# Optimization experiments

Hardware: AMD Instinct MI355X
Metric: run time of the kernel (lower is better)

## Reference

```python
import jax, jax.numpy as jnp
import numpy as np

# ----- problem dimensions (must match setup_inputs) -----
B = 50          # graphs per batch
NPG = 2000      # nodes per graph (equal-size graphs)
N = B * NPG     # total nodes = 100_000
D = 128         # in_channels
E = 600_000     # total edges
EA = 16         # edge_attr_dim
RATIO = 0.5
K = int(RATIO * NPG)  # nodes kept per graph = 1000
EPS = 1e-6


def setup_inputs() -> dict:
    key = jax.random.key(0)
    ks = jax.random.split(key, 12)
    x = jax.random.normal(ks[0], (N, D), jnp.float32)
    # edges constrained within graphs (each graph owns a contiguous node block)
    eg = jax.random.randint(ks[1], (E,), 0, B)
    src = eg * NPG + jax.random.randint(ks[2], (E,), 0, NPG)
    dst = eg * NPG + jax.random.randint(ks[3], (E,), 0, NPG)
    edge_index = jnp.stack([src, dst]).astype(jnp.int32)
    edge_attr = jax.random.normal(ks[4], (E, EA), jnp.float32)
    batch = (jnp.arange(N) // NPG).astype(jnp.int32)
    # feat_mlp: Linear(D,D) -> ReLU -> Linear(D,1)
    W1 = jax.random.normal(ks[5], (D, D), jnp.float32) / np.sqrt(D)
    b1 = jnp.zeros((D,), jnp.float32)
    W2 = jax.random.normal(ks[6], (D, 1), jnp.float32) / np.sqrt(D)
    b2 = jnp.zeros((1,), jnp.float32)
    # edge_mlp: Linear(EA,D) -> ReLU -> Linear(D,1)
    We1 = jax.random.normal(ks[7], (EA, D), jnp.float32) / np.sqrt(EA)
    be1 = jnp.zeros((D,), jnp.float32)
    We2 = jax.random.normal(ks[8], (D, 1), jnp.float32) / np.sqrt(D)
    be2 = jnp.zeros((1,), jnp.float32)
    view_weight = jnp.ones((3,), jnp.float32)
    return {"x": x, "edge_index": edge_index, "edge_attr": edge_attr,
            "batch": batch, "W1": W1, "b1": b1, "W2": W2, "b2": b2,
            "We1": We1, "be1": be1, "We2": We2, "be2": be2,
            "view_weight": view_weight}


def _standardize(v):
    # torch .std() is unbiased (ddof=1)
    return (v - v.mean()) / (jnp.std(v, ddof=1) + EPS)


def _scores(x, src, dst, edge_attr, W1, b1, W2, b2, We1, be1, We2, be2, vw):
    # edge weights: softplus(edge_mlp(edge_attr)) + eps
    ew = jax.nn.softplus((jax.nn.relu(edge_attr @ We1 + be1) @ We2 + be2)[:, 0]) + EPS
    deg_w = jnp.zeros((N,), x.dtype).at[src].add(ew)
    dis = jnp.where(deg_w > 0, deg_w ** -0.5, 0.0)
    norm = dis[src] * ew * dis[dst]                       # [E]
    x_diff = jnp.zeros_like(x).at[src].add(x[dst] * norm[:, None])  # [N,D]
    # view 1: structural (log degree)
    deg_c = jnp.zeros((N,), x.dtype).at[src].add(1.0)
    struct_score = _standardize(jnp.log(deg_c + 1.0))
    # view 2: feature MLP
    feat_raw = (jax.nn.relu(x @ W1 + b1) @ W2 + b2)[:, 0]
    feat_score = _standardize(feat_raw)
    # view 3: diffusion cosine similarity
    dot = jnp.sum(x * x_diff, axis=-1)
    cos = dot / ((jnp.linalg.norm(x, axis=-1) + EPS) *
                 (jnp.linalg.norm(x_diff, axis=-1) + EPS))
    diff_score = _standardize(cos)
    raw = jnp.stack([struct_score, feat_score, diff_score], axis=-1) @ vw
    return jax.nn.sigmoid(raw)                            # [N]


def reference(x, edge_index, edge_attr, batch, W1, b1, W2, b2,
              We1, be1, We2, be2, view_weight):
    src, dst = edge_index[0], edge_index[1]
    score = _scores(x, src, dst, edge_attr, W1, b1, W2, b2,
                    We1, be1, We2, be2, view_weight)
    # vectorized per-graph top-k (graphs are equal-size contiguous blocks)
    loc = jax.lax.top_k(score.reshape(B, NPG), K)[1]      # [B,K] local indices
    keep = (jnp.arange(B, dtype=loc.dtype)[:, None] * NPG + loc).reshape(-1)  # [B*K]
    node_mask = jnp.zeros((N,), bool).at[keep].set(True)
    new_id = jnp.full((N,), -1, jnp.int32).at[keep].set(
        jnp.arange(B * K, dtype=jnp.int32))
    e_mask = node_mask[src] & node_mask[dst]              # [E]
    out_edge_index = jnp.where(e_mask[None, :],
                               jnp.stack([new_id[src], new_id[dst]]), 0)
    out_edge_attr = jnp.where(e_mask[:, None], edge_attr, 0.0)
    out_x = x[keep] * score[keep][:, None]                # [B*K, D]
    out_batch = (jnp.arange(B * K) // K).astype(batch.dtype)
    return out_x, out_edge_index, out_edge_attr, out_batch, e_mask
```

## Files before the change

### kernel.cpp

```cpp
#include <hip/hip_runtime.h>
#include <math.h>

#define NN   100000
#define DD   128
#define EE   600000
#define EAD  16
#define BB   50
#define NPG  2000
#define KK   1000
#define NKEEP (BB*KK)

#define OFF_OEI    6400000
#define OFF_OEA    7600000
#define OFF_OBATCH 17200000
#define OFF_EMASK  17250000

#define NRED 240
#define SCAN_NB 98

#define EASTR 20
__global__ __launch_bounds__(256) void k_edge_mlp(
    const float* __restrict__ edge_attr, const int* __restrict__ src,
    const float* __restrict__ We1, const float* __restrict__ be1,
    const float* __restrict__ We2, const float* __restrict__ be2,
    float* __restrict__ ew, float* __restrict__ deg_w, float* __restrict__ deg_c)
{
    __shared__ float ea[256 * EASTR];
    __shared__ float wt[2048];
    __shared__ float b1s[128];
    __shared__ float w2s[128];
    int tid = threadIdx.x;
    int ebase = blockIdx.x * 256;

    if (tid < 128) {
        float tmp[16];
        #pragma unroll
        for (int k = 0; k < 16; k++) tmp[k] = We1[k * DD + tid];
        #pragma unroll
        for (int c = 0; c < 4; c++)
            *(float4*)(wt + tid * 16 + c * 4) =
                make_float4(tmp[4*c], tmp[4*c+1], tmp[4*c+2], tmp[4*c+3]);
        b1s[tid] = be1[tid];
        w2s[tid] = We2[tid];
    }
    #pragma unroll
    for (int it = 0; it < 4; it++) {
        int idx = tid + 256 * it;
        long long g = (long long)ebase * 4 + idx;
        long long maxg = (long long)EE * 4;
        if (g >= maxg) g = maxg - 1;
        float4 v = ((const float4*)edge_attr)[g];
        int le = idx >> 2, c = idx & 3;
        *(float4*)(ea + le * EASTR + c * 4) = v;
    }
    __syncthreads();

    float av[16];
    {
        const float* a = ea + tid * EASTR;
        float4 a0 = *(const float4*)(a);
        float4 a1 = *(const float4*)(a + 4);
        float4 a2 = *(const float4*)(a + 8);
        float4 a3 = *(const float4*)(a + 12);
        av[0]=a0.x; av[1]=a0.y; av[2]=a0.z; av[3]=a0.w;
        av[4]=a1.x; av[5]=a1.y; av[6]=a1.z; av[7]=a1.w;
        av[8]=a2.x; av[9]=a2.y; av[10]=a2.z; av[11]=a2.w;
        av[12]=a3.x; av[13]=a3.y; av[14]=a3.z; av[15]=a3.w;
    }

    float acc = 0.f;
    #pragma unroll 4
    for (int j = 0; j < DD; j++) {
        float4 w0 = *(const float4*)(wt + j * 16);
        float4 w1 = *(const float4*)(wt + j * 16 + 4);
        float4 w2 = *(const float4*)(wt + j * 16 + 8);
        float4 w3 = *(const float4*)(wt + j * 16 + 12);
        float h = b1s[j];
        h += av[0]*w0.x;  h += av[1]*w0.y;  h += av[2]*w0.z;  h += av[3]*w0.w;
        h += av[4]*w1.x;  h += av[5]*w1.y;  h += av[6]*w1.z;  h += av[7]*w1.w;
        h += av[8]*w2.x;  h += av[9]*w2.y;  h += av[10]*w2.z; h += av[11]*w2.w;
        h += av[12]*w3.x; h += av[13]*w3.y; h += av[14]*w3.z; h += av[15]*w3.w;
        acc += fmaxf(h, 0.f) * w2s[j];
    }

    int e = ebase + tid;
    if (e < EE) {
        float a = acc + be2[0];
        float sp = fmaxf(a, 0.f) + log1pf(expf(-fabsf(a)));
        float w = sp + 1e-6f;
        ew[e] = w;
        int s = src[e];
        atomicAdd(&deg_w[s], w);
        atomicAdd(&deg_c[s], 1.0f);
    }
}

__global__ __launch_bounds__(256) void k_dis(const float* __restrict__ deg_w,
                                             float* __restrict__ dis)
{
    int n = blockIdx.x * 256 + threadIdx.x;
    if (n >= NN) return;
    float d = deg_w[n];
    dis[n] = d > 0.f ? 1.f / sqrtf(d) : 0.f;
}

__global__ __launch_bounds__(1024) void k_scan_block(
    const float* __restrict__ deg_c, int* __restrict__ scanned,
    int* __restrict__ blocksums)
{
    __shared__ int s[1024];
    int i = blockIdx.x * 1024 + threadIdx.x;
    int c = (i < NN) ? (int)deg_c[i] : 0;
    s[threadIdx.x] = c;
    __syncthreads();
    for (int off = 1; off < 1024; off <<= 1) {
        int v = (threadIdx.x >= off) ? s[threadIdx.x - off] : 0;
        __syncthreads();
        s[threadIdx.x] += v;
        __syncthreads();
    }
    if (i < NN) scanned[i] = s[threadIdx.x] - c;
    if (threadIdx.x == 1023) blocksums[blockIdx.x] = s[1023];
}

__global__ __launch_bounds__(128) void k_scan_top(int* __restrict__ blocksums)
{
    __shared__ int s[128];
    int c = (threadIdx.x < SCAN_NB) ? blocksums[threadIdx.x] : 0;
    s[threadIdx.x] = c;
    __syncthreads();
    for (int off = 1; off < 128; off <<= 1) {
        int v = (threadIdx.x >= off) ? s[threadIdx.x - off] : 0;
        __syncthreads();
        s[threadIdx.x] += v;
        __syncthreads();
    }
    if (threadIdx.x < SCAN_NB) blocksums[threadIdx.x] = s[threadIdx.x] - c;
}

__global__ __launch_bounds__(256) void k_cursor(
    const int* __restrict__ scanned, const int* __restrict__ blocksums,
    int* __restrict__ rowstart, int* __restrict__ cur)
{
    int n = blockIdx.x * 256 + threadIdx.x;
    if (n >= NN) return;
    int st = scanned[n] + blocksums[n >> 10];
    rowstart[n] = st;
    cur[n] = st;
}

__global__ __launch_bounds__(256) void k_scatter(
    const int* __restrict__ src, const int* __restrict__ dst,
    const float* __restrict__ ew, const float* __restrict__ dis,
    int* __restrict__ cur, int* __restrict__ csr_dst, float* __restrict__ csr_w)
{
    int e = blockIdx.x * 256 + threadIdx.x;
    if (e >= EE) return;
    int s = src[e], d = dst[e];
    float w = dis[s] * ew[e] * dis[d];
    int pos = atomicAdd(&cur[s], 1);
    csr_dst[pos] = d;
    csr_w[pos] = w;
}

__global__ __launch_bounds__(256) void k_gather_cos(
    const int* __restrict__ rowstart, const float* __restrict__ deg_c,
    const int* __restrict__ csr_dst, const float* __restrict__ csr_w,
    const float* __restrict__ x, float* __restrict__ raw0, float* __restrict__ raw2)
{
    int blk = blockIdx.x;
    int node = ((blk & 7) * 3125 + (blk >> 3)) * 4 + (threadIdx.x >> 6);
    int lane = threadIdx.x & 63;
    if (node >= NN) return;
    int start = rowstart[node];
    int deg = (int)deg_c[node];
    const float2* xp = (const float2*)x;
    float2 xn = xp[(size_t)node * 64 + lane];
    float2 acc = {0.f, 0.f};
    for (int base = 0; base < deg; base += 64) {
        int rem = deg - base; if (rem > 64) rem = 64;
        int md = 0; float mw = 0.f;
        if (lane < rem) {
            md = csr_dst[start + base + lane];
            mw = csr_w[start + base + lane];
        }
        int e = 0;
        for (; e + 4 <= rem; e += 4) {
            int d0 = __shfl(md, e, 64),   d1 = __shfl(md, e+1, 64);
            int d2 = __shfl(md, e+2, 64), d3 = __shfl(md, e+3, 64);
            float w0 = __shfl(mw, e, 64),   w1 = __shfl(mw, e+1, 64);
            float w2 = __shfl(mw, e+2, 64), w3 = __shfl(mw, e+3, 64);
            float2 v0 = xp[(size_t)d0 * 64 + lane];
            float2 v1 = xp[(size_t)d1 * 64 + lane];
            float2 v2 = xp[(size_t)d2 * 64 + lane];
            float2 v3 = xp[(size_t)d3 * 64 + lane];
            acc.x += w0 * v0.x; acc.y += w0 * v0.y;
            acc.x += w1 * v1.x; acc.y += w1 * v1.y;
            acc.x += w2 * v2.x; acc.y += w2 * v2.y;
            acc.x += w3 * v3.x; acc.y += w3 * v3.y;
        }
        for (; e < rem; e++) {
            int d = __shfl(md, e, 64);
            float w = __shfl(mw, e, 64);
            float2 v = xp[(size_t)d * 64 + lane];
            acc.x += w * v.x; acc.y += w * v.y;
        }
    }
    float dot = xn.x * acc.x + xn.y * acc.y;
    float nx  = xn.x * xn.x + xn.y * xn.y;
    float nd  = acc.x * acc.x + acc.y * acc.y;
    #pragma unroll
    for (int off = 32; off; off >>= 1) {
        dot += __shfl_xor(dot, off, 64);
        nx  += __shfl_xor(nx,  off, 64);
        nd  += __shfl_xor(nd,  off, 64);
    }
    if (lane == 0) {
        raw2[node] = dot / ((sqrtf(nx) + 1e-6f) * (sqrtf(nd) + 1e-6f));
        raw0[node] = logf((float)deg + 1.0f);
    }
}

#define XSTR 132
__global__ __launch_bounds__(256) void k_node(
    const float* __restrict__ x,
    const float* __restrict__ W1, const float* __restrict__ b1,
    const float* __restrict__ W2, const float* __restrict__ b2,
    float* __restrict__ raw1)
{
    __shared__ float xs[64 * XSTR];
    int wave = threadIdx.x >> 6, lane = threadIdx.x & 63;
    int ng = lane >> 4, jg = lane & 15;
    int blockBase = blockIdx.x * 64;

    #pragma unroll
    for (int it = 0; it < 8; it++) {
        int s = threadIdx.x + 256 * it;
        int row = s >> 5, c4 = s & 31;
        int gn = blockBase + row; if (gn >= NN) gn = NN - 1;
        *(float4*)(xs + row * XSTR + c4 * 4) =
            *(const float4*)(x + (size_t)gn * DD + c4 * 4);
    }
    __syncthreads();

    const float* xw = xs + (wave * 16 + ng * 4) * XSTR;
    int j0 = jg * 8;
    float acc[4][8];
    #pragma unroll
    for (int i = 0; i < 4; i++)
        #pragma unroll
        for (int jj = 0; jj < 8; jj++) acc[i][jj] = 0.f;

    for (int k = 0; k < DD; k += 4) {
        float4 xv[4];
        #pragma unroll
        for (int i = 0; i < 4; i++) xv[i] = *(const float4*)(xw + i * XSTR + k);
        float4 wv[4][2];
        #pragma unroll
        for (int kk = 0; kk < 4; kk++) {
            wv[kk][0] = *(const float4*)(W1 + (k + kk) * DD + j0);
            wv[kk][1] = *(const float4*)(W1 + (k + kk) * DD + j0 + 4);
        }
        #pragma unroll
        for (int i = 0; i < 4; i++) {
            const float xe[4] = {xv[i].x, xv[i].y, xv[i].z, xv[i].w};
            #pragma unroll
            for (int kk = 0; kk < 4; kk++) {
                acc[i][0] += xe[kk] * wv[kk][0].x;
                acc[i][1] += xe[kk] * wv[kk][0].y;
                acc[i][2] += xe[kk] * wv[kk][0].z;
                acc[i][3] += xe[kk] * wv[kk][0].w;
                acc[i][4] += xe[kk] * wv[kk][1].x;
                acc[i][5] += xe[kk] * wv[kk][1].y;
                acc[i][6] += xe[kk] * wv[kk][1].z;
                acc[i][7] += xe[kk] * wv[kk][1].w;
            }
        }
    }

    float4 b1a = *(const float4*)(b1 + j0), b1b = *(const float4*)(b1 + j0 + 4);
    float4 w2a = *(const float4*)(W2 + j0), w2b = *(const float4*)(W2 + j0 + 4);
    const float b1v[8] = {b1a.x,b1a.y,b1a.z,b1a.w, b1b.x,b1b.y,b1b.z,b1b.w};
    const float w2v[8] = {w2a.x,w2a.y,w2a.z,w2a.w, w2b.x,w2b.y,w2b.z,w2b.w};
    float bias2 = b2[0];
    #pragma unroll
    for (int i = 0; i < 4; i++) {
        float p = 0.f;
        #pragma unroll
        for (int jj = 0; jj < 8; jj++)
            p += fmaxf(acc[i][jj] + b1v[jj], 0.f) * w2v[jj];
        p += __shfl_xor(p, 1, 64);
        p += __shfl_xor(p, 2, 64);
        p += __shfl_xor(p, 4, 64);
        p += __shfl_xor(p, 8, 64);
        int node = blockBase + wave * 16 + ng * 4 + i;
        if (jg == 0 && node < NN) raw1[node] = p + bias2;
    }
}

__global__ __launch_bounds__(256) void k_reduce(
    const float* __restrict__ r0, const float* __restrict__ r1,
    const float* __restrict__ r2, double* __restrict__ partials)
{
    __shared__ double sd[256];
    double s[6] = {0,0,0,0,0,0};
    for (int n = blockIdx.x * 256 + threadIdx.x; n < NN; n += 256 * NRED) {
        double v0 = r0[n], v1 = r1[n], v2 = r2[n];
        s[0] += v0; s[1] += v0*v0;
        s[2] += v1; s[3] += v1*v1;
        s[4] += v2; s[5] += v2*v2;
    }
    for (int q = 0; q < 6; q++) {
        sd[threadIdx.x] = s[q];
        __syncthreads();
        for (int off = 128; off; off >>= 1) {
            if (threadIdx.x < off) sd[threadIdx.x] += sd[threadIdx.x + off];
            __syncthreads();
        }
        if (threadIdx.x == 0) partials[blockIdx.x * 6 + q] = sd[0];
        __syncthreads();
    }
}

__global__ __launch_bounds__(256) void k_stats(const double* __restrict__ partials,
                                               float* __restrict__ stats)
{
    __shared__ double sd[256];
    __shared__ double sums[6];
    for (int q = 0; q < 6; q++) {
        sd[threadIdx.x] = (threadIdx.x < NRED) ? partials[threadIdx.x * 6 + q] : 0.0;
        __syncthreads();
        for (int off = 128; off; off >>= 1) {
            if (threadIdx.x < off) sd[threadIdx.x] += sd[threadIdx.x + off];
            __syncthreads();
        }
        if (threadIdx.x == 0) sums[q] = sd[0];
        __syncthreads();
    }
    if (threadIdx.x == 0) {
        for (int i = 0; i < 3; i++) {
            double sum = sums[2*i], sq = sums[2*i+1];
            double mean = sum / NN;
            double var = (sq - sum * sum / NN) / (NN - 1);
            double sdv = sqrt(var > 0 ? var : 0);
            stats[2*i]   = (float)mean;
            stats[2*i+1] = (float)(1.0 / (sdv + 1e-6));
        }
    }
}

__global__ __launch_bounds__(256) void k_score(
    const float* __restrict__ r0, const float* __restrict__ r1,
    const float* __restrict__ r2, const float* __restrict__ stats,
    const float* __restrict__ vw, float* __restrict__ score)
{
    int n = blockIdx.x * 256 + threadIdx.x;
    if (n >= NN) return;
    float z0 = (r0[n] - stats[0]) * stats[1];
    float z1 = (r1[n] - stats[2]) * stats[3];
    float z2 = (r2[n] - stats[4]) * stats[5];
    float r = z0 * vw[0] + z1 * vw[1] + z2 * vw[2];
    score[n] = 1.f / (1.f + expf(-r));
}

__global__ __launch_bounds__(1024) void k_topk(
    const float* __restrict__ score, int* __restrict__ keep,
    int* __restrict__ new_id, float* __restrict__ obatch)
{
    __shared__ unsigned long long keys[2048];
    int b = blockIdx.x;
    unsigned t = threadIdx.x;
    for (unsigned i = t; i < 2048; i += 1024) {
        unsigned long long kk = 0ull;
        if (i < NPG) {
            float sc = score[b * NPG + i];
            kk = ((unsigned long long)__float_as_uint(sc) << 32)
               | (unsigned long long)(0xFFFFFFFFu - i);
        }
        keys[i] = kk;
    }
    __syncthreads();
    for (unsigned k = 2; k <= 2048; k <<= 1) {
        for (unsigned j = k >> 1; j > 0; j >>= 1) {
            unsigned i = ((t & ~(j - 1)) << 1) | (t & (j - 1));
            unsigned p = i | j;
            unsigned long long a = keys[i], c = keys[p];
            bool up = ((i & k) == 0);
            if ((a < c) == up) { keys[i] = c; keys[p] = a; }
            __syncthreads();
        }
    }
    if (t < KK) {
        unsigned long long kk = keys[t];
        unsigned li = 0xFFFFFFFFu - (unsigned)(kk & 0xFFFFFFFFu);
        int node = b * NPG + (int)li;
        int j = b * KK + (int)t;
        keep[j] = node;
        new_id[node] = j;
        obatch[j] = (float)b;
    }
}

__global__ __launch_bounds__(128) void k_outx(
    const float* __restrict__ x, const float* __restrict__ score,
    const int* __restrict__ keep, float* __restrict__ out_x)
{
    int j = blockIdx.x;
    int node = keep[j];
    float s = score[node];
    out_x[(size_t)j * DD + threadIdx.x] = x[(size_t)node * DD + threadIdx.x] * s;
}

__global__ __launch_bounds__(256) void k_edges(
    const int* __restrict__ src, const int* __restrict__ dst,
    const int* __restrict__ new_id, float* __restrict__ oei,
    float* __restrict__ emask)
{
    int e = blockIdx.x * 256 + threadIdx.x;
    if (e >= EE) return;
    int ns = new_id[src[e]], nd = new_id[dst[e]];
    bool m = (ns >= 0) && (nd >= 0);
    oei[e]      = m ? (float)ns : 0.f;
    oei[EE + e] = m ? (float)nd : 0.f;
    emask[e]    = m ? 1.f : 0.f;
}

__global__ __launch_bounds__(256) void k_attr(
    const float* __restrict__ edge_attr, const float* __restrict__ emask,
    float* __restrict__ oea)
{
    int idx = blockIdx.x * 256 + threadIdx.x;
    if (idx >= EE * 4) return;
    int e = idx >> 2;
    float m = emask[e];
    float4 v = ((const float4*)edge_attr)[idx];
    float4 o; o.x = v.x*m; o.y = v.y*m; o.z = v.z*m; o.w = v.w*m;
    ((float4*)oea)[idx] = o;
}

extern "C" void kernel_launch(void* const* d_in, const int* in_sizes, int n_in,
                              void* d_out, int out_size, void* d_ws, size_t ws_size,
                              hipStream_t stream) {
    const float* x         = (const float*)d_in[0];
    const int*   edge_idx  = (const int*)d_in[1];
    const float* edge_attr = (const float*)d_in[2];
    const float* W1  = (const float*)d_in[4];
    const float* b1  = (const float*)d_in[5];
    const float* W2  = (const float*)d_in[6];
    const float* b2  = (const float*)d_in[7];
    const float* We1 = (const float*)d_in[8];
    const float* be1 = (const float*)d_in[9];
    const float* We2 = (const float*)d_in[10];
    const float* be2 = (const float*)d_in[11];
    const float* vw  = (const float*)d_in[12];

    const int* src = edge_idx;
    const int* dst = edge_idx + EE;

    float* out    = (float*)d_out;
    float* out_x  = out;
    float* oei    = out + OFF_OEI;
    float* oea    = out + OFF_OEA;
    float* obatch = out + OFF_OBATCH;
    float* emask  = out + OFF_EMASK;

    int*   csr_dst   = (int*)(out + 12800000);
    float* csr_w     = out + 13400000;
    int*   rowstart  = (int*)(out + 14000000);
    int*   cur       = (int*)(out + 14100000);
    int*   scanned   = (int*)(out + 14200000);
    int*   blocksums = (int*)(out + 14300000);

    float* ws     = (float*)d_ws;
    float* ew     = ws;
    float* deg_w  = ws + 600000;
    float* deg_c  = ws + 700000;
    float* dis    = ws + 800000;
    float* score  = ws + 900000;
    float* raw0   = ws + 1000000;
    float* raw1   = ws + 1100000;
    float* raw2   = ws + 1200000;
    int*   keep   = (int*)(ws + 1300000);
    int*   new_id = (int*)(ws + 1350000);
    double* partials = (double*)(ws + 1450000);
    float* stats  = ws + 1450000 + 2 * 6 * NRED;

    hipMemsetAsync(deg_w, 0, 2 * NN * sizeof(float), stream);
    hipMemsetAsync(new_id, 0xFF, NN * sizeof(int), stream);

    k_edge_mlp<<<(EE + 255) / 256, 256, 0, stream>>>(edge_attr, src, We1, be1,
                                                     We2, be2, ew, deg_w, deg_c);
    k_dis<<<(NN + 255) / 256, 256, 0, stream>>>(deg_w, dis);
    k_scan_block<<<SCAN_NB, 1024, 0, stream>>>(deg_c, scanned, blocksums);
    k_scan_top<<<1, 128, 0, stream>>>(blocksums);
    k_cursor<<<(NN + 255) / 256, 256, 0, stream>>>(scanned, blocksums, rowstart, cur);
    k_scatter<<<(EE + 255) / 256, 256, 0, stream>>>(src, dst, ew, dis, cur, csr_dst, csr_w);
    k_gather_cos<<<(NN * 64 + 255) / 256, 256, 0, stream>>>(rowstart, deg_c, csr_dst,
                                                            csr_w, x, raw0, raw2);
    k_node<<<(NN + 63) / 64, 256, 0, stream>>>(x, W1, b1, W2, b2, raw1);
    k_reduce<<<NRED, 256, 0, stream>>>(raw0, raw1, raw2, partials);
    k_stats<<<1, 256, 0, stream>>>(partials, stats);
    k_score<<<(NN + 255) / 256, 256, 0, stream>>>(raw0, raw1, raw2, stats, vw, score);
    k_topk<<<BB, 1024, 0, stream>>>(score, keep, new_id, obatch);
    k_outx<<<NKEEP, 128, 0, stream>>>(x, score, keep, out_x);
    k_edges<<<(EE + 255) / 256, 256, 0, stream>>>(src, dst, new_id, oei, emask);
    k_attr<<<(EE * 4 + 255) / 256, 256, 0, stream>>>(edge_attr, emask, oea);
}
```

Baseline: 430.4 us.

## Pre-pack edge MLP weights and compute two edges per thread from global

A tiny prep kernel packs We1 columns, be1 and We2 into a 20-float-per-hidden-unit layout in scratch output memory. The edge MLP kernel then drops its shared-memory staging and reads these weights directly from global, where all lanes hit the same address and the cache serves them. Each thread now handles two edges, so every weight fetch feeds twice as many FMAs. This trades shared-memory staging and barrier cost for higher register pressure and one extra kernel launch.

New measurement: 444.6 us. +3.3%, slower.

```diff
diff --git a/kernel.cpp b/kernel.cpp
--- a/kernel.cpp
+++ b/kernel.cpp
@@ -18,78 +18,83 @@
 #define NRED 240
 #define SCAN_NB 98
 
-#define EASTR 20
+__global__ __launch_bounds__(128) void k_wprep(
+    const float* __restrict__ We1, const float* __restrict__ be1,
+    const float* __restrict__ We2, float* __restrict__ wp)
+{
+    int j = threadIdx.x;
+    #pragma unroll
+    for (int k = 0; k < EAD; k++) wp[j * 20 + k] = We1[k * DD + j];
+    wp[j * 20 + 16] = be1[j];
+    wp[j * 20 + 17] = We2[j];
+    wp[j * 20 + 18] = 0.f;
+    wp[j * 20 + 19] = 0.f;
+}
+
 __global__ __launch_bounds__(256) void k_edge_mlp(
     const float* __restrict__ edge_attr, const int* __restrict__ src,
-    const float* __restrict__ We1, const float* __restrict__ be1,
-    const float* __restrict__ We2, const float* __restrict__ be2,
+    const float* __restrict__ wp, const float* __restrict__ be2,
     float* __restrict__ ew, float* __restrict__ deg_w, float* __restrict__ deg_c)
 {
-    __shared__ float ea[256 * EASTR];
-    __shared__ float wt[2048];
-    __shared__ float b1s[128];
-    __shared__ float w2s[128];
     int tid = threadIdx.x;
-    int ebase = blockIdx.x * 256;
-
-    if (tid < 128) {
-        float tmp[16];
-        #pragma unroll
-        for (int k = 0; k < 16; k++) tmp[k] = We1[k * DD + tid];
-        #pragma unroll
-        for (int c = 0; c < 4; c++)
-            *(float4*)(wt + tid * 16 + c * 4) =
-                make_float4(tmp[4*c], tmp[4*c+1], tmp[4*c+2], tmp[4*c+3]);
-        b1s[tid] = be1[tid];
-        w2s[tid] = We2[tid];
-    }
-    #pragma unroll
-    for (int it = 0; it < 4; it++) {
-        int idx = tid + 256 * it;
-        long long g = (long long)ebase * 4 + idx;
-        long long maxg = (long long)EE * 4;
-        if (g >= maxg) g = maxg - 1;
-        float4 v = ((const float4*)edge_attr)[g];
-        int le = idx >> 2, c = idx & 3;
-        *(float4*)(ea + le * EASTR + c * 4) = v;
-    }
-    __syncthreads();
-
-    float av[16];
-    {
-        const float* a = ea + tid * EASTR;
-        float4 a0 = *(const float4*)(a);
-        float4 a1 = *(const float4*)(a + 4);
-        float4 a2 = *(const float4*)(a + 8);
-        float4 a3 = *(const float4*)(a + 12);
-        av[0]=a0.x; av[1]=a0.y; av[2]=a0.z; av[3]=a0.w;
-        av[4]=a1.x; av[5]=a1.y; av[6]=a1.z; av[7]=a1.w;
-        av[8]=a2.x; av[9]=a2.y; av[10]=a2.z; av[11]=a2.w;
-        av[12]=a3.x; av[13]=a3.y; av[14]=a3.z; av[15]=a3.w;
-    }
-
-    float acc = 0.f;
+    int ebase = blockIdx.x * 512;
+    int e0 = ebase + tid;
+    int e1 = ebase + 256 + tid;
+    int le0 = (e0 < EE) ? e0 : (EE - 1);
+    int le1 = (e1 < EE) ? e1 : (EE - 1);
+
+    const float4* ea4 = (const float4*)edge_attr;
+    float a0[16], a1[16];
+    #pragma unroll
+    for (int c = 0; c < 4; c++) {
+        float4 v = ea4[(size_t)le0 * 4 + c];
+        a0[4*c] = v.x; a0[4*c+1] = v.y; a0[4*c+2] = v.z; a0[4*c+3] = v.w;
+    }
+    #pragma unroll
+    for (int c = 0; c < 4; c++) {
+        float4 v = ea4[(size_t)le1 * 4 + c];
+        a1[4*c] = v.x; a1[4*c+1] = v.y; a1[4*c+2] = v.z; a1[4*c+3] = v.w;
+    }
+
+    float acc0 = 0.f, acc1 = 0.f;
     #pragma unroll 4
     for (int j = 0; j < DD; j++) {
-        float4 w0 = *(const float4*)(wt + j * 16);
-        float4 w1 = *(const float4*)(wt + j * 16 + 4);
-        float4 w2 = *(const float4*)(wt + j * 16 + 8);
-        float4 w3 = *(const float4*)(wt + j * 16 + 12);
-        float h = b1s[j];
-        h += av[0]*w0.x;  h += av[1]*w0.y;  h += av[2]*w0.z;  h += av[3]*w0.w;
-        h += av[4]*w1.x;  h += av[5]*w1.y;  h += av[6]*w1.z;  h += av[7]*w1.w;
-        h += av[8]*w2.x;  h += av[9]*w2.y;  h += av[10]*w2.z; h += av[11]*w2.w;
-        h += av[12]*w3.x; h += av[13]*w3.y; h += av[14]*w3.z; h += av[15]*w3.w;
-        acc += fmaxf(h, 0.f) * w2s[j];
-    }
-
-    int e = ebase + tid;
-    if (e < EE) {
-        float a = acc + be2[0];
+        const float* w = wp + j * 20;
+        float4 w0 = *(const float4*)(w);
+        float4 w1 = *(const float4*)(w + 4);
+        float4 w2 = *(const float4*)(w + 8);
+        float4 w3 = *(const float4*)(w + 12);
+        float bj  = w[16];
+        float v2  = w[17];
+        float h0 = bj, h1 = bj;
+        h0 += a0[0]*w0.x;  h0 += a0[1]*w0.y;  h0 += a0[2]*w0.z;  h0 += a0[3]*w0.w;
+        h0 += a0[4]*w1.x;  h0 += a0[5]*w1.y;  h0 += a0[6]*w1.z;  h0 += a0[7]*w1.w;
+        h0 += a0[8]*w2.x;  h0 += a0[9]*w2.y;  h0 += a0[10]*w2.z; h0 += a0[11]*w2.w;
+        h0 += a0[12]*w3.x; h0 += a0[13]*w3.y; h0 += a0[14]*w3.z; h0 += a0[15]*w3.w;
+        h1 += a1[0]*w0.x;  h1 += a1[1]*w0.y;  h1 += a1[2]*w0.z;  h1 += a1[3]*w0.w;
+        h1 += a1[4]*w1.x;  h1 += a1[5]*w1.y;  h1 += a1[6]*w1.z;  h1 += a1[7]*w1.w;
+        h1 += a1[8]*w2.x;  h1 += a1[9]*w2.y;  h1 += a1[10]*w2.z; h1 += a1[11]*w2.w;
+        h1 += a1[12]*w3.x; h1 += a1[13]*w3.y; h1 += a1[14]*w3.z; h1 += a1[15]*w3.w;
+        acc0 += fmaxf(h0, 0.f) * v2;
+        acc1 += fmaxf(h1, 0.f) * v2;
+    }
+
+    float bias2 = be2[0];
+    if (e0 < EE) {
+        float a = acc0 + bias2;
         float sp = fmaxf(a, 0.f) + log1pf(expf(-fabsf(a)));
         float w = sp + 1e-6f;
-        ew[e] = w;
-        int s = src[e];
+        ew[e0] = w;
+        int s = src[e0];
+        atomicAdd(&deg_w[s], w);
+        atomicAdd(&deg_c[s], 1.0f);
+    }
+    if (e1 < EE) {
+        float a = acc1 + bias2;
+        float sp = fmaxf(a, 0.f) + log1pf(expf(-fabsf(a)));
+        float w = sp + 1e-6f;
+        ew[e1] = w;
+        int s = src[e1];
         atomicAdd(&deg_w[s], w);
         atomicAdd(&deg_c[s], 1.0f);
     }
@@ -470,6 +475,7 @@
     int*   cur       = (int*)(out + 14100000);
     int*   scanned   = (int*)(out + 14200000);
     int*   blocksums = (int*)(out + 14300000);
+    float* wp        = out + 14400000;
 
     float* ws     = (float*)d_ws;
     float* ew     = ws;
@@ -488,8 +494,9 @@
     hipMemsetAsync(deg_w, 0, 2 * NN * sizeof(float), stream);
     hipMemsetAsync(new_id, 0xFF, NN * sizeof(int), stream);
 
-    k_edge_mlp<<<(EE + 255) / 256, 256, 0, stream>>>(edge_attr, src, We1, be1,
-                                                     We2, be2, ew, deg_w, deg_c);
+    k_wprep<<<1, 128, 0, stream>>>(We1, be1, We2, wp);
+    k_edge_mlp<<<(EE + 511) / 512, 256, 0, stream>>>(edge_attr, src, wp, be2,
+                                                     ew, deg_w, deg_c);
     k_dis<<<(NN + 255) / 256, 256, 0, stream>>>(deg_w, dis);
     k_scan_block<<<SCAN_NB, 1024, 0, stream>>>(deg_c, scanned, blocksums);
     k_scan_top<<<1, 128, 0, stream>>>(blocksums);
```

## Register-tile edge MLP across lanes with shuffle reduction over hidden units

Applied to the files above, without the earlier changes.

Rewrites the edge MLP kernel so each block handles 64 edges. Each lane computes a 4-edge by 8-hidden-unit register tile, reading weights straight from global/L1 instead of staging the whole weight matrix in shared memory, and the output dot product is reduced across 16 lanes with shuffles. This cuts the redundant per-thread 128x16 loop and the heavy shared-memory weight reads, but launches four times more blocks and adds shuffle and partial-lane work.

Result: no change. 434.1 us (+0.8%).

```diff
diff --git a/kernel.cpp b/kernel.cpp
--- a/kernel.cpp
+++ b/kernel.cpp
@@ -18,80 +18,89 @@
 #define NRED 240
 #define SCAN_NB 98
 
-#define EASTR 20
+#define EB 64
 __global__ __launch_bounds__(256) void k_edge_mlp(
     const float* __restrict__ edge_attr, const int* __restrict__ src,
     const float* __restrict__ We1, const float* __restrict__ be1,
     const float* __restrict__ We2, const float* __restrict__ be2,
     float* __restrict__ ew, float* __restrict__ deg_w, float* __restrict__ deg_c)
 {
-    __shared__ float ea[256 * EASTR];
-    __shared__ float wt[2048];
-    __shared__ float b1s[128];
-    __shared__ float w2s[128];
+    __shared__ float ea[EB * 20];
     int tid = threadIdx.x;
-    int ebase = blockIdx.x * 256;
-
-    if (tid < 128) {
-        float tmp[16];
-        #pragma unroll
-        for (int k = 0; k < 16; k++) tmp[k] = We1[k * DD + tid];
-        #pragma unroll
-        for (int c = 0; c < 4; c++)
-            *(float4*)(wt + tid * 16 + c * 4) =
-                make_float4(tmp[4*c], tmp[4*c+1], tmp[4*c+2], tmp[4*c+3]);
-        b1s[tid] = be1[tid];
-        w2s[tid] = We2[tid];
-    }
+    int wave = tid >> 6, lane = tid & 63;
+    int ng = lane >> 4, jg = lane & 15;
+    int ebase = blockIdx.x * EB;
+
+    {
+        int row = tid >> 2, c = tid & 3;
+        *(float4*)(ea + row * 20 + c * 4) =
+            *(const float4*)(edge_attr + (size_t)(ebase + row) * EAD + c * 4);
+    }
+    __syncthreads();
+
+    int j0 = jg * 8;
+    const float* xw = ea + (wave * 16 + ng * 4) * 20;
+
+    float acc[4][8];
     #pragma unroll
-    for (int it = 0; it < 4; it++) {
-        int idx = tid + 256 * it;
-        long long g = (long long)ebase * 4 + idx;
-        long long maxg = (long long)EE * 4;
-        if (g >= maxg) g = maxg - 1;
-        float4 v = ((const float4*)edge_attr)[g];
-        int le = idx >> 2, c = idx & 3;
-        *(float4*)(ea + le * EASTR + c * 4) = v;
-    }
-    __syncthreads();
-
-    float av[16];
-    {
-        const float* a = ea + tid * EASTR;
-        float4 a0 = *(const float4*)(a);
-        float4 a1 = *(const float4*)(a + 4);
-        float4 a2 = *(const float4*)(a + 8);
-        float4 a3 = *(const float4*)(a + 12);
-        av[0]=a0.x; av[1]=a0.y; av[2]=a0.z; av[3]=a0.w;
-        av[4]=a1.x; av[5]=a1.y; av[6]=a1.z; av[7]=a1.w;
-        av[8]=a2.x; av[9]=a2.y; av[10]=a2.z; av[11]=a2.w;
-        av[12]=a3.x; av[13]=a3.y; av[14]=a3.z; av[15]=a3.w;
-    }
-
-    float acc = 0.f;
-    #pragma unroll 4
-    for (int j = 0; j < DD; j++) {
-        float4 w0 = *(const float4*)(wt + j * 16);
-        float4 w1 = *(const float4*)(wt + j * 16 + 4);
-        float4 w2 = *(const float4*)(wt + j * 16 + 8);
-        float4 w3 = *(const float4*)(wt + j * 16 + 12);
-        float h = b1s[j];
-        h += av[0]*w0.x;  h += av[1]*w0.y;  h += av[2]*w0.z;  h += av[3]*w0.w;
-        h += av[4]*w1.x;  h += av[5]*w1.y;  h += av[6]*w1.z;  h += av[7]*w1.w;
-        h += av[8]*w2.x;  h += av[9]*w2.y;  h += av[10]*w2.z; h += av[11]*w2.w;
-        h += av[12]*w3.x; h += av[13]*w3.y; h += av[14]*w3.z; h += av[15]*w3.w;
-        acc += fmaxf(h, 0.f) * w2s[j];
-    }
-
-    int e = ebase + tid;
-    if (e < EE) {
-        float a = acc + be2[0];
-        float sp = fmaxf(a, 0.f) + log1pf(expf(-fabsf(a)));
-        float w = sp + 1e-6f;
-        ew[e] = w;
-        int s = src[e];
-        atomicAdd(&deg_w[s], w);
-        atomicAdd(&deg_c[s], 1.0f);
+    for (int i = 0; i < 4; i++)
+        #pragma unroll
+        for (int jj = 0; jj < 8; jj++) acc[i][jj] = 0.f;
+
+    #pragma unroll 1
+    for (int k = 0; k < EAD; k += 4) {
+        float4 xv[4];
+        #pragma unroll
+        for (int i = 0; i < 4; i++) xv[i] = *(const float4*)(xw + i * 20 + k);
+        float4 wv[4][2];
+        #pragma unroll
+        for (int kk = 0; kk < 4; kk++) {
+            wv[kk][0] = *(const float4*)(We1 + (k + kk) * DD + j0);
+            wv[kk][1] = *(const float4*)(We1 + (k + kk) * DD + j0 + 4);
+        }
+        #pragma unroll
+        for (int i = 0; i < 4; i++) {
+            const float xe[4] = {xv[i].x, xv[i].y, xv[i].z, xv[i].w};
+            #pragma unroll
+            for (int kk = 0; kk < 4; kk++) {
+                acc[i][0] += xe[kk] * wv[kk][0].x;
+                acc[i][1] += xe[kk] * wv[kk][0].y;
+                acc[i][2] += xe[kk] * wv[kk][0].z;
+                acc[i][3] += xe[kk] * wv[kk][0].w;
+                acc[i][4] += xe[kk] * wv[kk][1].x;
+                acc[i][5] += xe[kk] * wv[kk][1].y;
+                acc[i][6] += xe[kk] * wv[kk][1].z;
+                acc[i][7] += xe[kk] * wv[kk][1].w;
+            }
+        }
+    }
+
+    float4 b1a = *(const float4*)(be1 + j0), b1b = *(const float4*)(be1 + j0 + 4);
+    float4 w2a = *(const float4*)(We2 + j0), w2b = *(const float4*)(We2 + j0 + 4);
+    const float b1v[8] = {b1a.x,b1a.y,b1a.z,b1a.w, b1b.x,b1b.y,b1b.z,b1b.w};
+    const float w2v[8] = {w2a.x,w2a.y,w2a.z,w2a.w, w2b.x,w2b.y,w2b.z,w2b.w};
+    float bias2 = be2[0];
+
+    #pragma unroll
+    for (int i = 0; i < 4; i++) {
+        float p = 0.f;
+        #pragma unroll
+        for (int jj = 0; jj < 8; jj++)
+            p += fmaxf(acc[i][jj] + b1v[jj], 0.f) * w2v[jj];
+        p += __shfl_xor(p, 1, 64);
+        p += __shfl_xor(p, 2, 64);
+        p += __shfl_xor(p, 4, 64);
+        p += __shfl_xor(p, 8, 64);
+        if (jg == 0) {
+            int e = ebase + wave * 16 + ng * 4 + i;
+            float a = p + bias2;
+            float sp = fmaxf(a, 0.f) + log1pf(expf(-fabsf(a)));
+            float w = sp + 1e-6f;
+            ew[e] = w;
+            int s = src[e];
+            atomicAdd(&deg_w[s], w);
+            atomicAdd(&deg_c[s], 1.0f);
+        }
     }
 }
 
@@ -488,8 +497,8 @@
     hipMemsetAsync(deg_w, 0, 2 * NN * sizeof(float), stream);
     hipMemsetAsync(new_id, 0xFF, NN * sizeof(int), stream);
 
-    k_edge_mlp<<<(EE + 255) / 256, 256, 0, stream>>>(edge_attr, src, We1, be1,
-                                                     We2, be2, ew, deg_w, deg_c);
+    k_edge_mlp<<<EE / EB, 256, 0, stream>>>(edge_attr, src, We1, be1,
+                                            We2, be2, ew, deg_w, deg_c);
     k_dis<<<(NN + 255) / 256, 256, 0, stream>>>(deg_w, dis);
     k_scan_block<<<SCAN_NB, 1024, 0, stream>>>(deg_c, scanned, blocksums);
     k_scan_top<<<1, 128, 0, stream>>>(blocksums);
```
